# Kernel tuning notes

Hardware: AMD Instinct MI355X
Metric: run time of the kernel (lower is better)

## Reference

```python
import jax, jax.numpy as jnp
import numpy as np

NEG_INF = -jnp.inf


def setup_inputs() -> dict:
    key = jax.random.key(0)
    ks = jax.random.split(key, 6)
    B, S, D, DK = 8, 2048, 1024, 128
    x = jax.random.normal(ks[0], (B, S, D), dtype=jnp.float32)
    context = jax.random.normal(ks[1], (B, S, D), dtype=jnp.float32)
    # torch nn.Linear weights: [out_features, in_features]
    Wq = jax.random.normal(ks[2], (DK, D), dtype=jnp.float32) * 0.02
    Wk = jax.random.normal(ks[3], (DK, D), dtype=jnp.float32) * 0.02
    Wv = jax.random.normal(ks[4], (DK, D), dtype=jnp.float32) * 0.02
    # valid lengths in [S//2, S] so every row has at least one valid key
    batch_lengths = jax.random.randint(ks[5], (B,), S // 2, S + 1, dtype=jnp.int32)
    return {
        "x": x,
        "context": context,
        "Wq": Wq,
        "Wk": Wk,
        "Wv": Wv,
        "batch_lengths": batch_lengths,
        "max_len": S,
        "decoding": 1,
    }


def reference(x, context, Wq, Wk, Wv, batch_lengths, max_len, decoding):
    B, S, D = x.shape
    dk = Wq.shape[0]
    pos = jnp.arange(S)
    # outputMask: 1.0 for t < length, else 0.0; broadcast over feature dim dk
    valid = pos[None, :] < batch_lengths[:, None]            # [B, S]
    mask = valid[:, :, None].astype(x.dtype)                 # [B, S, 1] (broadcast to dk)
    Q = jnp.einsum('bsd,kd->bsk', context, Wq) * mask        # [B, S, dk]
    K = jnp.einsum('bsd,kd->bsk', context, Wk) * mask
    V = jnp.einsum('bsd,kd->bsk', x, Wv) * mask
    energy = jnp.einsum('bqk,bjk->bqj', Q, K)                # [B, S, S]
    # attnMask: -inf at padded key positions (j >= length)
    key_pad = ~valid                                         # [B, S]
    energy = jnp.where(key_pad[:, None, :], NEG_INF, energy)
    if decoding:
        # causal: energy[:, i, j] = -inf for j > i (the python double loop)
        causal = pos[:, None] < pos[None, :]                 # [S, S], True above diag
        energy = jnp.where(causal[None, :, :], NEG_INF, energy)
    score = jax.nn.softmax(energy / jnp.sqrt(jnp.asarray(dk, x.dtype)), axis=-1)
    return jnp.einsum('bqj,bjk->bqk', score, V)              # [B, S, dk]
```

## Files before the change

kernel.cpp:

```cpp
#include <hip/hip_runtime.h>
#include <hip/hip_bf16.h>
#include <hip/hip_fp16.h>

#define BB 8
#define SS 2048
#define DD 1024
#define DKK 128
#define N_ITEMS 2560

using bf16x8  = __attribute__((ext_vector_type(8))) __bf16;
using floatx4 = __attribute__((ext_vector_type(4))) float;
using intx4   = __attribute__((ext_vector_type(4))) int;
using halfx8  = __attribute__((ext_vector_type(8))) _Float16;

__device__ __forceinline__ void lds16(const void* g, void* l) {
    __builtin_amdgcn_global_load_lds((const __attribute__((address_space(1))) void*)g,
                                     (__attribute__((address_space(3))) void*)l, 16, 0, 0);
}

__device__ __forceinline__ int pack2(float a, float b) {
    union { __bf16 h; unsigned short u; } ua, ub;
    ua.h = (__bf16)a; ub.h = (__bf16)b;
    return (int)(ua.u | ((unsigned)ub.u << 16));
}

__global__ __launch_bounds__(256) void convw_kernel(
    const float* __restrict__ Wq, const float* __restrict__ Wk,
    const float* __restrict__ Wv, __bf16* __restrict__ Wt)
{
    const int z = blockIdx.y;
    const float* W = (z == 0) ? Wq : (z == 1) ? Wk : Wv;
    const int t  = blockIdx.x * 256 + threadIdx.x;
    const int n  = t >> 7;
    const int k0 = (t & 127) * 8;
    float4 f0 = *(const float4*)(W + n * DD + k0);
    float4 f1 = *(const float4*)(W + n * DD + k0 + 4);
    bf16x8 v;
    v[0]=(__bf16)f0.x; v[1]=(__bf16)f0.y; v[2]=(__bf16)f0.z; v[3]=(__bf16)f0.w;
    v[4]=(__bf16)f1.x; v[5]=(__bf16)f1.y; v[6]=(__bf16)f1.z; v[7]=(__bf16)f1.w;
    const int kb  = (k0 >> 3) & 7;
    const int kbs = kb ^ (n & 7);
    *(bf16x8*)(Wt + (size_t)z * 131072 + ((k0 >> 6) * 128 + n) * 64 + kbs * 8) = v;
}

__global__ __launch_bounds__(256, 4) void proj_kernel(
    const float* __restrict__ x, const float* __restrict__ ctx,
    const __bf16* __restrict__ Wt, const int* __restrict__ lengths,
    __bf16* __restrict__ Qb, __bf16* __restrict__ Kb, __bf16* __restrict__ Vt)
{
    __shared__ __align__(16) __bf16 SH[10496];
    __bf16* Abuf = SH;
    __bf16* Wl   = SH + 2304;
    __bf16* T    = SH;

    const int z  = blockIdx.x >> 9;
    const int m0 = (blockIdx.x & 511) * 32;
    const int b   = m0 >> 11;
    const int s0  = m0 & (SS - 1);
    const int len = lengths[b];
    if (s0 >= len) return;

    const int tid  = threadIdx.x;
    const int wave = tid >> 6;
    const int lane = tid & 63;
    const int quad = lane >> 4;
    const int l16  = lane & 15;
    const int wm   = wave >> 1;
    const int wn   = wave & 1;

    const float*  A  = (z == 2) ? x : ctx;
    const __bf16* W0 = Wt + (size_t)z * 131072;

    const int r    = tid >> 3;
    const int kseg = (tid & 7) * 8;
    const float* Ab = A + (size_t)(m0 + r) * DD + kseg;

    floatx4 acc[4];
#pragma unroll
    for (int nt = 0; nt < 4; ++nt) acc[nt] = (floatx4){0.f,0.f,0.f,0.f};

    float4 pf0 = *(const float4*)Ab;
    float4 pf1 = *(const float4*)(Ab + 4);

    for (int t = 0; t < 16; ++t) {
        __syncthreads();
        {
            bf16x8 cv;
            cv[0]=(__bf16)pf0.x; cv[1]=(__bf16)pf0.y; cv[2]=(__bf16)pf0.z; cv[3]=(__bf16)pf0.w;
            cv[4]=(__bf16)pf1.x; cv[5]=(__bf16)pf1.y; cv[6]=(__bf16)pf1.z; cv[7]=(__bf16)pf1.w;
            *(bf16x8*)&Abuf[r * 72 + kseg] = cv;
        }
#pragma unroll
        for (int i = 0; i < 4; ++i) {
            const int c = wave * 4 + i;
            lds16(W0 + (size_t)t * 8192 + c * 512 + lane * 8, Wl + c * 512);
        }
        if (t < 15) {
            const float* ap = Ab + (t + 1) * 64;
            pf0 = *(const float4*)ap;
            pf1 = *(const float4*)(ap + 4);
        }
        __syncthreads();

#pragma unroll
        for (int kh = 0; kh < 2; ++kh) {
            bf16x8 af = *(const bf16x8*)&Abuf[(wm*16 + l16) * 72 + kh*32 + quad*8];
            const int kb = kh * 4 + quad;
#pragma unroll
            for (int nt = 0; nt < 4; ++nt) {
                const int n = wn * 64 + nt * 16 + l16;
                bf16x8 w = *(const bf16x8*)&Wl[n * 64 + ((kb ^ (n & 7)) << 3)];
                acc[nt] = __builtin_amdgcn_mfma_f32_16x16x32_bf16(af, w, acc[nt], 0, 0, 0);
            }
        }
    }

    if (z < 2) {
        __bf16* D = z ? Kb : Qb;
#pragma unroll
        for (int rr = 0; rr < 4; ++rr) {
            const int row = m0 + wm*16 + quad*4 + rr;
            const float mk = ((row & (SS - 1)) < len) ? 1.f : 0.f;
#pragma unroll
            for (int nt = 0; nt < 4; ++nt)
                D[(size_t)row * DKK + wn*64 + nt*16 + l16] = (__bf16)(acc[nt][rr] * mk);
        }
    } else {
        __syncthreads();
#pragma unroll
        for (int nt = 0; nt < 4; ++nt)
#pragma unroll
            for (int rr = 0; rr < 4; ++rr) {
                const int s = wm*16 + quad*4 + rr;
                const int n = wn*64 + nt*16 + l16;
                const float mk = (s0 + s < len) ? 1.f : 0.f;
                T[n * 40 + s] = (__bf16)(acc[nt][rr] * mk);
            }
        __syncthreads();
        const int n = tid >> 1, h = tid & 1;
        __bf16* dst = Vt + (size_t)b * DKK * SS + (size_t)n * SS + s0 + h * 16;
        *(bf16x8*)dst       = *(const bf16x8*)&T[n * 40 + h * 16];
        *(bf16x8*)(dst + 8) = *(const bf16x8*)&T[n * 40 + h * 16 + 8];
    }
}

__global__ __launch_bounds__(256) void vmean_kernel(
    const __bf16* __restrict__ Vt, const int* __restrict__ lengths,
    float* __restrict__ Vmean)
{
    const int b   = blockIdx.x >> 3;
    const int g3  = blockIdx.x & 7;
    const int len = lengths[b];
    const int tid = threadIdx.x;
    const int n   = g3 * 16 + (tid >> 4);
    const int sl  = (tid & 15) * 128;
    const __bf16* src = Vt + (size_t)b * DKK * SS + (size_t)n * SS + sl;
    float s = 0.f;
#pragma unroll
    for (int i = 0; i < 16; ++i) {
        bf16x8 v = *(const bf16x8*)(src + i * 8);
#pragma unroll
        for (int j = 0; j < 8; ++j)
            s += (sl + i * 8 + j < len) ? (float)v[j] : 0.f;
    }
#pragma unroll
    for (int off = 1; off < 16; off <<= 1)
        s += __shfl_xor(s, off, 64);
    if ((tid & 15) == 0) Vmean[b * DKK + n] = s / (float)len;
}

__global__ __launch_bounds__(64) void attn_part_kernel(
    const __bf16* __restrict__ Qb, const __bf16* __restrict__ Kb,
    const __bf16* __restrict__ Vt, const int* __restrict__ lengths,
    _Float16* __restrict__ Opart, float* __restrict__ Lpart)
{
    const int f  = N_ITEMS - 1 - blockIdx.x;
    const int b  = f / 320;
    const int r0 = f - b * 320;
    const int g  = (r0 < 32) ? 0 : (r0 < 96) ? 1 : (r0 < 192) ? 2 : 3;
    const int r_ = r0 - 16 * g * (g + 1);
    const int t0 = 32 * g + r_ / (g + 1);
    const int kc = r_ - (t0 - 32 * g) * (g + 1);

    const int qw  = t0 * 16;
    const int len = lengths[b];
    if (qw >= len) return;
    const int jmax = min(qw + 16, len);
    const int jlo  = kc * 512;
    if (jlo >= jmax) return;
    const int jhi = min(jlo + 512, jmax);

    const int lane = threadIdx.x;
    const int quad = lane >> 4;
    const int l16  = lane & 15;

    const __bf16* Qbase = Qb + (size_t)(b * SS + qw) * DKK;
    const __bf16* Kbase = Kb + (size_t)b * SS * DKK;
    const __bf16* Vbase = Vt + (size_t)b * DKK * SS;

    bf16x8 qfrag[4];
#pragma unroll
    for (int cc = 0; cc < 4; ++cc)
        qfrag[cc] = *(const bf16x8*)(Qbase + (size_t)l16 * DKK + cc * 32 + quad * 8);

    floatx4 oacc[8];
#pragma unroll
    for (int nt = 0; nt < 8; ++nt) oacc[nt] = (floatx4){0.f,0.f,0.f,0.f};
    float lsum = 0.f;
    const float scale = 0.08838834764831845f;
    const int   iq    = qw + l16;

    auto loadK = [&](int j0, bf16x8* kf) {
#pragma unroll
        for (int jt = 0; jt < 2; ++jt)
#pragma unroll
            for (int cc = 0; cc < 4; ++cc)
                kf[jt * 4 + cc] = *(const bf16x8*)(
                    Kbase + (size_t)(j0 + jt*16 + l16) * DKK + cc*32 + quad*8);
    };
    auto body = [&](int j0, const bf16x8* kf) {
        bf16x8 vf[8];
#pragma unroll
        for (int nt = 0; nt < 8; ++nt)
            vf[nt] = *(const bf16x8*)(Vbase + (size_t)(nt*16 + l16) * SS + j0 + quad*8);

        floatx4 st[2];
#pragma unroll
        for (int jt = 0; jt < 2; ++jt) {
            st[jt] = (floatx4){0.f,0.f,0.f,0.f};
#pragma unroll
            for (int cc = 0; cc < 4; ++cc)
                st[jt] = __builtin_amdgcn_mfma_f32_16x16x32_bf16(
                    kf[jt*4 + cc], qfrag[cc], st[jt], 0, 0, 0);
        }
        int pk[2][2];
#pragma unroll
        for (int jt = 0; jt < 2; ++jt) {
            float p[4];
#pragma unroll
            for (int rr = 0; rr < 4; ++rr) {
                const int j = j0 + jt*16 + quad*4 + rr;
                p[rr] = (j > iq || j >= len) ? 0.f : __expf(st[jt][rr] * scale - 8.f);
                lsum += p[rr];
            }
            pk[jt][0] = pack2(p[0], p[1]);
            pk[jt][1] = pack2(p[2], p[3]);
        }
        const int a0 = (((quad & 1) << 5) + l16) << 2;
        const int a1 = a0 + 64;
        const int r00 = __builtin_amdgcn_ds_bpermute(a0, pk[0][0]);
        const int r01 = __builtin_amdgcn_ds_bpermute(a0, pk[0][1]);
        const int r02 = __builtin_amdgcn_ds_bpermute(a0, pk[1][0]);
        const int r03 = __builtin_amdgcn_ds_bpermute(a0, pk[1][1]);
        const int r10 = __builtin_amdgcn_ds_bpermute(a1, pk[0][0]);
        const int r11 = __builtin_amdgcn_ds_bpermute(a1, pk[0][1]);
        const int r12 = __builtin_amdgcn_ds_bpermute(a1, pk[1][0]);
        const int r13 = __builtin_amdgcn_ds_bpermute(a1, pk[1][1]);
        const bool hi = quad >= 2;
        union { intx4 i; bf16x8 h; } u;
        u.i = (intx4){ hi ? r02 : r00, hi ? r03 : r01,
                       hi ? r12 : r10, hi ? r13 : r11 };
#pragma unroll
        for (int nt = 0; nt < 8; ++nt)
            oacc[nt] = __builtin_amdgcn_mfma_f32_16x16x32_bf16(u.h, vf[nt], oacc[nt], 0, 0, 0);
    };

    bf16x8 kf0[8], kf1[8];
    int j0 = jlo;
    loadK(j0, kf0);
    while (true) {
        if (j0 + 32 < jhi) loadK(j0 + 32, kf1);
        body(j0, kf0);
        j0 += 32; if (j0 >= jhi) break;
        if (j0 + 32 < jhi) loadK(j0 + 32, kf0);
        body(j0, kf1);
        j0 += 32; if (j0 >= jhi) break;
    }

    lsum += __shfl_xor(lsum, 16, 64);
    lsum += __shfl_xor(lsum, 32, 64);
    if (lane < 16) Lpart[f * 16 + l16] = lsum;
#pragma unroll
    for (int nt = 0; nt < 8; ++nt)
#pragma unroll
        for (int rr = 0; rr < 4; ++rr)
            Opart[(size_t)f * 2048 + (quad*4 + rr) * 128 + nt*16 + l16] =
                (_Float16)oacc[nt][rr];
}

__global__ __launch_bounds__(256) void attn_fin_kernel(
    const _Float16* __restrict__ Opart, const float* __restrict__ Lpart,
    const float* __restrict__ Vmean, const int* __restrict__ lengths,
    float* __restrict__ out)
{
    const int tile = blockIdx.x;
    const int b    = tile >> 7;
    const int t0   = tile & 127;
    const int qw   = t0 * 16;
    const int len  = lengths[b];
    const int row  = threadIdx.x >> 4;
    const int c8   = (threadIdx.x & 15) * 8;
    float* op = out + (size_t)(b * SS + qw + row) * DKK + c8;

    if (qw >= len) {
#pragma unroll
        for (int k = 0; k < 8; ++k) op[k] = Vmean[b * DKK + c8 + k];
        return;
    }

    const int g     = t0 >> 5;
    const int jmax  = min(qw + 16, len);
    const int nv    = min(g + 1, (jmax + 511) >> 9);
    const int fbase = b * 320 + 16 * g * (g + 1) + (t0 - 32 * g) * (g + 1);

    float l = 0.f;
    float o[8] = {0.f,0.f,0.f,0.f,0.f,0.f,0.f,0.f};
    for (int i = 0; i < nv; ++i) {
        l += Lpart[(fbase + i) * 16 + row];
        halfx8 h8 = *(const halfx8*)(Opart + (size_t)(fbase + i) * 2048 + row * 128 + c8);
#pragma unroll
        for (int k = 0; k < 8; ++k) o[k] += (float)h8[k];
    }
    const float inv = 1.f / l;
#pragma unroll
    for (int k = 0; k < 8; ++k) op[k] = o[k] * inv;
}

extern "C" void kernel_launch(void* const* d_in, const int* in_sizes, int n_in,
                              void* d_out, int out_size, void* d_ws, size_t ws_size,
                              hipStream_t stream) {
    const float* x   = (const float*)d_in[0];
    const float* ctx = (const float*)d_in[1];
    const float* Wq  = (const float*)d_in[2];
    const float* Wk  = (const float*)d_in[3];
    const float* Wv  = (const float*)d_in[4];
    const int* lengths = (const int*)d_in[5];
    float* out = (float*)d_out;

    char* ws = (char*)d_ws;
    __bf16*   Wt = (__bf16*)ws;
    __bf16*   Qb = (__bf16*)(ws + 786432);
    __bf16*   Kb = (__bf16*)(ws + 4980736);
    __bf16*   Vt = (__bf16*)(ws + 9175040);
    float*    Lp = (float*)  (ws + 13369344);
    _Float16* Op = (_Float16*)(ws + 13533184);
    float*    Vm = (float*)  (ws + 24018944);

    convw_kernel<<<dim3(64, 3), 256, 0, stream>>>(Wq, Wk, Wv, Wt);
    proj_kernel<<<1536, 256, 0, stream>>>(x, ctx, Wt, lengths, Qb, Kb, Vt);
    vmean_kernel<<<64, 256, 0, stream>>>(Vt, lengths, Vm);
    attn_part_kernel<<<N_ITEMS, 64, 0, stream>>>(Qb, Kb, Vt, lengths, Op, Lp);
    attn_fin_kernel<<<1024, 256, 0, stream>>>(Op, Lp, Vm, lengths, out);
}
```

Baseline: 247.5 us.

## Fuse Q/K projections per block and drop the separate V-mean path

The projection kernel now computes Q and K in the same block, so each context tile is converted and staged in LDS once and multiplied by both weight tiles. The grid shrinks from 1536 to 1024 blocks, and the block holds a second LDS weight buffer and a second set of accumulators. The vmean kernel and the padded-query shortcut in the finalize kernel are removed. Padded query tiles now go through the normal partial-attention path using masked (zero) Q, which adds attention work for those rows. This relies on Qb rows past the valid length being zero, but the projection kernel still returns early for those blocks and never writes them.

```diff
diff --git a/kernel.cpp b/kernel.cpp
--- a/kernel.cpp
+++ b/kernel.cpp
@@ -48,13 +48,14 @@
     const __bf16* __restrict__ Wt, const int* __restrict__ lengths,
     __bf16* __restrict__ Qb, __bf16* __restrict__ Kb, __bf16* __restrict__ Vt)
 {
-    __shared__ __align__(16) __bf16 SH[10496];
+    __shared__ __align__(16) __bf16 SH[18688];
     __bf16* Abuf = SH;
-    __bf16* Wl   = SH + 2304;
+    __bf16* Wl0  = SH + 2304;
+    __bf16* Wl1  = SH + 10496;
     __bf16* T    = SH;
 
-    const int z  = blockIdx.x >> 9;
-    const int m0 = (blockIdx.x & 511) * 32;
+    const int isV = blockIdx.x >= 512;
+    const int m0  = (isV ? blockIdx.x - 512 : blockIdx.x) * 32;
     const int b   = m0 >> 11;
     const int s0  = m0 & (SS - 1);
     const int len = lengths[b];
@@ -68,16 +69,20 @@
     const int wm   = wave >> 1;
     const int wn   = wave & 1;
 
-    const float*  A  = (z == 2) ? x : ctx;
-    const __bf16* W0 = Wt + (size_t)z * 131072;
+    const float*  A  = isV ? x : ctx;
+    const __bf16* W0 = isV ? (Wt + 262144) : Wt;
+    const __bf16* W1 = Wt + 131072;
 
     const int r    = tid >> 3;
     const int kseg = (tid & 7) * 8;
     const float* Ab = A + (size_t)(m0 + r) * DD + kseg;
 
-    floatx4 acc[4];
-#pragma unroll
-    for (int nt = 0; nt < 4; ++nt) acc[nt] = (floatx4){0.f,0.f,0.f,0.f};
+    floatx4 acc0[4], acc1[4];
+#pragma unroll
+    for (int nt = 0; nt < 4; ++nt) {
+        acc0[nt] = (floatx4){0.f,0.f,0.f,0.f};
+        acc1[nt] = (floatx4){0.f,0.f,0.f,0.f};
+    }
 
     float4 pf0 = *(const float4*)Ab;
     float4 pf1 = *(const float4*)(Ab + 4);
@@ -93,7 +98,9 @@
 #pragma unroll
         for (int i = 0; i < 4; ++i) {
             const int c = wave * 4 + i;
-            lds16(W0 + (size_t)t * 8192 + c * 512 + lane * 8, Wl + c * 512);
+            lds16(W0 + (size_t)t * 8192 + c * 512 + lane * 8, Wl0 + c * 512);
+            if (!isV)
+                lds16(W1 + (size_t)t * 8192 + c * 512 + lane * 8, Wl1 + c * 512);
         }
         if (t < 15) {
             const float* ap = Ab + (t + 1) * 64;
@@ -109,21 +116,28 @@
 #pragma unroll
             for (int nt = 0; nt < 4; ++nt) {
                 const int n = wn * 64 + nt * 16 + l16;
-                bf16x8 w = *(const bf16x8*)&Wl[n * 64 + ((kb ^ (n & 7)) << 3)];
-                acc[nt] = __builtin_amdgcn_mfma_f32_16x16x32_bf16(af, w, acc[nt], 0, 0, 0);
+                const int off = n * 64 + ((kb ^ (n & 7)) << 3);
+                bf16x8 w0 = *(const bf16x8*)&Wl0[off];
+                acc0[nt] = __builtin_amdgcn_mfma_f32_16x16x32_bf16(af, w0, acc0[nt], 0, 0, 0);
+                if (!isV) {
+                    bf16x8 w1 = *(const bf16x8*)&Wl1[off];
+                    acc1[nt] = __builtin_amdgcn_mfma_f32_16x16x32_bf16(af, w1, acc1[nt], 0, 0, 0);
+                }
             }
         }
     }
 
-    if (z < 2) {
-        __bf16* D = z ? Kb : Qb;
+    if (!isV) {
 #pragma unroll
         for (int rr = 0; rr < 4; ++rr) {
             const int row = m0 + wm*16 + quad*4 + rr;
             const float mk = ((row & (SS - 1)) < len) ? 1.f : 0.f;
 #pragma unroll
-            for (int nt = 0; nt < 4; ++nt)
-                D[(size_t)row * DKK + wn*64 + nt*16 + l16] = (__bf16)(acc[nt][rr] * mk);
+            for (int nt = 0; nt < 4; ++nt) {
+                const int col = wn*64 + nt*16 + l16;
+                Qb[(size_t)row * DKK + col] = (__bf16)(acc0[nt][rr] * mk);
+                Kb[(size_t)row * DKK + col] = (__bf16)(acc1[nt][rr] * mk);
+            }
         }
     } else {
         __syncthreads();
@@ -134,7 +148,7 @@
                 const int s = wm*16 + quad*4 + rr;
                 const int n = wn*64 + nt*16 + l16;
                 const float mk = (s0 + s < len) ? 1.f : 0.f;
-                T[n * 40 + s] = (__bf16)(acc[nt][rr] * mk);
+                T[n * 40 + s] = (__bf16)(acc0[nt][rr] * mk);
             }
         __syncthreads();
         const int n = tid >> 1, h = tid & 1;
@@ -142,31 +156,6 @@
         *(bf16x8*)dst       = *(const bf16x8*)&T[n * 40 + h * 16];
         *(bf16x8*)(dst + 8) = *(const bf16x8*)&T[n * 40 + h * 16 + 8];
     }
-}
-
-__global__ __launch_bounds__(256) void vmean_kernel(
-    const __bf16* __restrict__ Vt, const int* __restrict__ lengths,
-    float* __restrict__ Vmean)
-{
-    const int b   = blockIdx.x >> 3;
-    const int g3  = blockIdx.x & 7;
-    const int len = lengths[b];
-    const int tid = threadIdx.x;
-    const int n   = g3 * 16 + (tid >> 4);
-    const int sl  = (tid & 15) * 128;
-    const __bf16* src = Vt + (size_t)b * DKK * SS + (size_t)n * SS + sl;
-    float s = 0.f;
-#pragma unroll
-    for (int i = 0; i < 16; ++i) {
-        bf16x8 v = *(const bf16x8*)(src + i * 8);
-#pragma unroll
-        for (int j = 0; j < 8; ++j)
-            s += (sl + i * 8 + j < len) ? (float)v[j] : 0.f;
-    }
-#pragma unroll
-    for (int off = 1; off < 16; off <<= 1)
-        s += __shfl_xor(s, off, 64);
-    if ((tid & 15) == 0) Vmean[b * DKK + n] = s / (float)len;
 }
 
 __global__ __launch_bounds__(64) void attn_part_kernel(
@@ -184,7 +173,6 @@
 
     const int qw  = t0 * 16;
     const int len = lengths[b];
-    if (qw >= len) return;
     const int jmax = min(qw + 16, len);
     const int jlo  = kc * 512;
     if (jlo >= jmax) return;
@@ -290,8 +278,7 @@
 
 __global__ __launch_bounds__(256) void attn_fin_kernel(
     const _Float16* __restrict__ Opart, const float* __restrict__ Lpart,
-    const float* __restrict__ Vmean, const int* __restrict__ lengths,
-    float* __restrict__ out)
+    const int* __restrict__ lengths, float* __restrict__ out)
 {
     const int tile = blockIdx.x;
     const int b    = tile >> 7;
@@ -301,12 +288,6 @@
     const int row  = threadIdx.x >> 4;
     const int c8   = (threadIdx.x & 15) * 8;
     float* op = out + (size_t)(b * SS + qw + row) * DKK + c8;
-
-    if (qw >= len) {
-#pragma unroll
-        for (int k = 0; k < 8; ++k) op[k] = Vmean[b * DKK + c8 + k];
-        return;
-    }
 
     const int g     = t0 >> 5;
     const int jmax  = min(qw + 16, len);
@@ -344,11 +325,9 @@
     __bf16*   Vt = (__bf16*)(ws + 9175040);
     float*    Lp = (float*)  (ws + 13369344);
     _Float16* Op = (_Float16*)(ws + 13533184);
-    float*    Vm = (float*)  (ws + 24018944);
 
     convw_kernel<<<dim3(64, 3), 256, 0, stream>>>(Wq, Wk, Wv, Wt);
-    proj_kernel<<<1536, 256, 0, stream>>>(x, ctx, Wt, lengths, Qb, Kb, Vt);
-    vmean_kernel<<<64, 256, 0, stream>>>(Vt, lengths, Vm);
+    proj_kernel<<<1024, 256, 0, stream>>>(x, ctx, Wt, lengths, Qb, Kb, Vt);
     attn_part_kernel<<<N_ITEMS, 64, 0, stream>>>(Qb, Kb, Vt, lengths, Op, Lp);
-    attn_fin_kernel<<<1024, 256, 0, stream>>>(Op, Lp, Vm, lengths, out);
-}
+    attn_fin_kernel<<<1024, 256, 0, stream>>>(Op, Lp, lengths, out);
+}
```

New measurement: 282.7 us. +14.3%, slower.
